# Kernel tuning notes

Measured on AMD Instinct MI355X. Metric: run time of the kernel, lower is better.

The kernel has to match this reference:

```python
import jax, jax.numpy as jnp
import numpy as np

B, L, D_IN, H, TAGS = 16, 128, 512, 256, 45


def setup_inputs() -> dict:
    key = jax.random.key(0)
    ks = jax.random.split(key, 10)
    s = 0.02
    return {
        "contextualized": jax.random.normal(ks[0], (B, L, D_IN), jnp.float32),
        "sentence_lengths": jax.random.randint(ks[1], (B,), 64, L + 1, jnp.int32),
        "desired_arcs": jax.random.randint(ks[2], (B, L), 0, L + 1, jnp.int32),
        "desired_labels": jax.random.randint(ks[3], (B, L), 0, TAGS, jnp.int32),
        "W1": jax.random.normal(ks[4], (D_IN, H), jnp.float32) * s,
        "b1": jnp.zeros((H,), jnp.float32),
        "root": jax.random.normal(ks[5], (H,), jnp.float32) * s,
        "Wp": jax.random.normal(ks[6], (2 * H, H), jnp.float32) * s,
        "bp": jnp.zeros((H,), jnp.float32),
        "W_arc": jax.random.normal(ks[7], (H, 1), jnp.float32) * s,
        "b_arc": jnp.zeros((1,), jnp.float32),
        "W_lab": jax.random.normal(ks[8], (H, TAGS), jnp.float32) * s,
        "b_lab": jnp.zeros((TAGS,), jnp.float32),
    }


def _forward(contextualized, sentence_lengths, desired_arcs, desired_labels,
             W1, b1, root, Wp, bp, W_arc, b_arc, W_lab, b_lab):
    b, l, _ = contextualized.shape
    h = W1.shape[1]
    # token representations: dense + relu
    hidden = jax.nn.relu(contextualized @ W1 + b1)                      # [B,L,H]
    # prepend learned root vector
    root_t = jnp.broadcast_to(root, (b, 1, h))
    cwr = jnp.concatenate([root_t, hidden], axis=1)                     # [B,L+1,H]
    # pairs dense: concat([tile_a, tile_b]) @ Wp == hidden@Wa + cwr@Wb (broadcast-add)
    Wa, Wb = Wp[:h], Wp[h:]
    pre = (hidden @ Wa)[:, :, None, :] + (cwr @ Wb)[:, None, :, :] + bp
    pairs_repr = jax.nn.relu(pre)                                       # [B,L,L+1,H]
    # valid-token mask from sentence lengths
    mask = (jnp.arange(l)[None, :] < sentence_lengths[:, None]).astype(jnp.float32)
    denom = jnp.maximum(mask.sum(), 1.0)
    # UAS: arc logits over L+1 head candidates, softmax CE vs gold arcs
    arc_logits = jnp.squeeze(pairs_repr @ W_arc, -1) + b_arc[0]         # [B,L,L+1]
    arc_logp = jax.nn.log_softmax(arc_logits, axis=-1)
    arc_ce = -jnp.take_along_axis(arc_logp, desired_arcs[:, :, None], axis=-1)[..., 0]
    uas_loss = jnp.sum(arc_ce * mask) / denom
    # LAS: select pair repr at gold arc, dense -> tag logits, softmax CE
    sel = jnp.take_along_axis(pairs_repr, desired_arcs[:, :, None, None].astype(jnp.int32)
                              .repeat(1, axis=2), axis=2)[:, :, 0, :]   # [B,L,H]
    label_logits = sel @ W_lab + b_lab                                  # [B,L,TAGS]
    lab_logp = jax.nn.log_softmax(label_logits, axis=-1)
    lab_ce = -jnp.take_along_axis(lab_logp, desired_labels[:, :, None], axis=-1)[..., 0]
    las_loss = jnp.sum(lab_ce * mask) / denom
    return (uas_loss + las_loss) * 0.5


def reference(contextualized, sentence_lengths, desired_arcs, desired_labels,
              W1, b1, root, Wp, bp, W_arc, b_arc, W_lab, b_lab):
    return _forward(contextualized, sentence_lengths, desired_arcs, desired_labels,
                    W1, b1, root, Wp, bp, W_arc, b_arc, W_lab, b_lab)
```

## Files before the change

### kernel.cpp

```cpp
#include <hip/hip_runtime.h>
#include <math.h>

#define NB 16
#define NL 128
#define DIN 512
#define NH 256
#define NTAGS 45
#define NM (NB*NL)
#define NJ (NL+1)

#define H_OFF     0
#define U_OFF     (2*NM*NH)
#define HV_OFF    (3*NM*NH)
#define VROOT_OFF (4*NM*NH)
#define ACC_OFF   (VROOT_OFF + NH)

__global__ __launch_bounds__(256) void gemm_hidden(
    const float* __restrict__ A,
    const float* __restrict__ W,
    const float* __restrict__ Wp,
    const float* __restrict__ root,
    float* __restrict__ h,
    float* __restrict__ vroot,
    float* __restrict__ accum)
{
    __shared__ float As[2][16][36];
    __shared__ float Bs[2][16][68];
    __shared__ float part[4][64];
    int m0 = blockIdx.x * 32;
    int n0 = blockIdx.y * 64;
    int kbase = blockIdx.z * 256;
    int tid = threadIdx.x;
    if (blockIdx.x == 0 && blockIdx.y == 0 && blockIdx.z == 0 && tid == 0) {
        accum[0] = 0.f;
        ((int*)accum)[1] = 0;
    }
    int lm = tid >> 2, lk = (tid & 3) * 4;
    int bk = tid >> 4, bn = (tid & 15) * 4;
    int tm = tid >> 4, tn = tid & 15;
    float acc[2][4] = {{0.f}};
    float4 a_r, b_r;

    auto LOADK = [&](int c) {
        int k0 = kbase + c * 16;
        if (tid < 128)
            a_r = *(const float4*)&A[(size_t)(m0 + lm) * DIN + k0 + lk];
        b_r = *(const float4*)&W[(size_t)(k0 + bk) * NH + n0 + bn];
    };
    auto WRITE = [&](int buf) {
        if (tid < 128) {
            As[buf][lk + 0][lm] = a_r.x; As[buf][lk + 1][lm] = a_r.y;
            As[buf][lk + 2][lm] = a_r.z; As[buf][lk + 3][lm] = a_r.w;
        }
        *(float4*)&Bs[buf][bk][bn] = b_r;
    };

    LOADK(0);
    WRITE(0);
    LOADK(1);
    __syncthreads();
    for (int c = 0; c < 16; ++c) {
        int buf = c & 1;
        #pragma unroll
        for (int kk = 0; kk < 16; kk++) {
            float2 a2 = *(const float2*)&As[buf][kk][tm * 2];
            float4 bv = *(const float4*)&Bs[buf][kk][tn * 4];
            float ar[2] = {a2.x, a2.y};
            float br[4] = {bv.x, bv.y, bv.z, bv.w};
            #pragma unroll
            for (int r = 0; r < 2; r++)
                #pragma unroll
                for (int cc = 0; cc < 4; cc++)
                    acc[r][cc] = fmaf(ar[r], br[cc], acc[r][cc]);
        }
        if (c < 15) {
            WRITE(buf ^ 1);
            if (c < 14) LOADK(c + 2);
            __syncthreads();
        }
    }
    float* hz = h + (size_t)blockIdx.z * NM * NH;
    int col = n0 + tn * 4;
    #pragma unroll
    for (int r = 0; r < 2; r++) {
        int row = m0 + tm * 2 + r;
        *(float4*)&hz[(size_t)row * NH + col] =
            make_float4(acc[r][0], acc[r][1], acc[r][2], acc[r][3]);
    }

    if (blockIdx.x == 63 && blockIdx.z == 1) {
        __syncthreads();
        int vcol = n0 + (tid & 63);
        int kc = tid >> 6;
        float p = 0.f;
        #pragma unroll 8
        for (int c = kc * 64; c < kc * 64 + 64; c++)
            p += root[c] * Wp[(size_t)(NH + c) * NH + vcol];
        part[kc][tid & 63] = p;
        __syncthreads();
        if (tid < 64)
            vroot[n0 + tid] = part[0][tid] + part[1][tid]
                            + part[2][tid] + part[3][tid];
    }
}

__global__ __launch_bounds__(256) void gemm_uv(
    const float* __restrict__ h,
    const float* __restrict__ b1,
    const float* __restrict__ Wp,
    const float* __restrict__ bp,
    float* __restrict__ u,
    float* __restrict__ hv)
{
    __shared__ float As[2][16][68];
    __shared__ float Bs[2][16][36];
    int m0 = blockIdx.x * 64;
    int n0 = blockIdx.y * 32;
    int tid = threadIdx.x;
    bool isU = (n0 < NH);
    int arow = tid >> 2, akq = (tid & 3) * 4;
    int bk = tid >> 3, bn = (tid & 7) * 4;
    int tm = tid >> 3, tn = tid & 7;
    float acc[2][4] = {{0.f}};
    float4 ha_r, hb_r, bi_r, b_r;

    auto LOADK = [&](int c) {
        int k0 = c * 16;
        size_t base = (size_t)(m0 + arow) * NH + k0 + akq;
        ha_r = *(const float4*)&h[base];
        hb_r = *(const float4*)&h[base + (size_t)NM * NH];
        bi_r = *(const float4*)&b1[k0 + akq];
        if (tid < 128) {
            int ck = k0 + bk;
            if (isU) b_r = *(const float4*)&Wp[(size_t)ck * NH + n0 + bn];
            else     b_r = *(const float4*)&Wp[(size_t)(NH + ck) * NH + (n0 - NH) + bn];
        }
    };
    auto WRITE = [&](int buf) {
        As[buf][akq + 0][arow] = fmaxf(ha_r.x + hb_r.x + bi_r.x, 0.f);
        As[buf][akq + 1][arow] = fmaxf(ha_r.y + hb_r.y + bi_r.y, 0.f);
        As[buf][akq + 2][arow] = fmaxf(ha_r.z + hb_r.z + bi_r.z, 0.f);
        As[buf][akq + 3][arow] = fmaxf(ha_r.w + hb_r.w + bi_r.w, 0.f);
        if (tid < 128)
            *(float4*)&Bs[buf][bk][bn] = b_r;
    };

    LOADK(0);
    WRITE(0);
    LOADK(1);
    __syncthreads();
    for (int c = 0; c < 16; ++c) {
        int buf = c & 1;
        #pragma unroll
        for (int kk = 0; kk < 16; kk++) {
            float2 a2 = *(const float2*)&As[buf][kk][tm * 2];
            float4 bv = *(const float4*)&Bs[buf][kk][tn * 4];
            float ar[2] = {a2.x, a2.y};
            float br[4] = {bv.x, bv.y, bv.z, bv.w};
            #pragma unroll
            for (int r = 0; r < 2; r++)
                #pragma unroll
                for (int cc = 0; cc < 4; cc++)
                    acc[r][cc] = fmaf(ar[r], br[cc], acc[r][cc]);
        }
        if (c < 15) {
            WRITE(buf ^ 1);
            if (c < 14) LOADK(c + 2);
            __syncthreads();
        }
    }
    if (isU) {
        int col = n0 + tn * 4;
        float4 bb = *(const float4*)&bp[col];
        #pragma unroll
        for (int r = 0; r < 2; r++) {
            int row = m0 + tm * 2 + r;
            *(float4*)&u[(size_t)row * NH + col] = make_float4(
                acc[r][0] + bb.x, acc[r][1] + bb.y,
                acc[r][2] + bb.z, acc[r][3] + bb.w);
        }
    } else {
        int col = (n0 - NH) + tn * 4;
        #pragma unroll
        for (int r = 0; r < 2; r++) {
            int row = m0 + tm * 2 + r;
            *(float4*)&hv[(size_t)row * NH + col] = make_float4(
                acc[r][0], acc[r][1], acc[r][2], acc[r][3]);
        }
    }
}

#define NBLK (NB*16)

__global__ __launch_bounds__(512) void score_loss_kernel(
    const float* __restrict__ u, const float* __restrict__ hv,
    const float* __restrict__ vroot, const float* __restrict__ W_arc,
    const float* __restrict__ W_lab, const float* __restrict__ b_lab,
    const int* __restrict__ slens, const int* __restrict__ arcs,
    const int* __restrict__ labels,
    float* __restrict__ accum, float* __restrict__ out)
{
    __shared__ float2 v2_s[32][129];
    __shared__ float2 u2_s[8][128];
    __shared__ float2 wa2_s[128];
    __shared__ float2 sel2_s[32][9];
    __shared__ float  ce_s[8];
    __shared__ int    arc_s[8], lab_s[8];

    int bb = blockIdx.x;
    int i0 = blockIdx.y * 8;
    int tid = threadIdx.x;
    int w = tid >> 6;
    int lane = tid & 63;
    int slen = slens[bb];

    if (i0 < slen) {
        {
            int r = tid >> 6, kq = (tid & 63) * 4;
            float4 a4 = *(const float4*)&u[(size_t)(bb * NL + i0 + r) * NH + kq];
            u2_s[r][(kq >> 1) + 0] = make_float2(a4.x, a4.y);
            u2_s[r][(kq >> 1) + 1] = make_float2(a4.z, a4.w);
        }
        if (tid < 128)
            wa2_s[tid] = *(const float2*)&W_arc[tid * 2];
        if (tid < 8) {
            int rg = bb * NL + i0 + tid;
            arc_s[tid] = arcs[rg];
            lab_s[tid] = labels[rg];
        }

        float4 vr[5];
        auto VLOAD = [&](int c) {
            int k0 = c * 64;
            #pragma unroll
            for (int s = 0; s < 5; ++s) {
                int idx = tid + s * 512;
                if (idx < NJ * 16) {
                    int j = idx >> 4, kq = (idx & 15) * 4;
                    const float* src = (j == 0) ? (vroot + k0 + kq)
                        : (hv + (size_t)(bb * NL + j - 1) * NH + k0 + kq);
                    vr[s] = *(const float4*)src;
                }
            }
        };
        auto VWRITE = [&]() {
            #pragma unroll
            for (int s = 0; s < 5; ++s) {
                int idx = tid + s * 512;
                if (idx < NJ * 16) {
                    int j = idx >> 4, kq = (idx & 15) * 4;
                    v2_s[(kq >> 1) + 0][j] = make_float2(vr[s].x, vr[s].y);
                    v2_s[(kq >> 1) + 1][j] = make_float2(vr[s].z, vr[s].w);
                }
            }
        };

        float acc1 = 0.f, acc2 = 0.f, s128 = 0.f, lacc = 0.f;

        VLOAD(0);
        for (int c = 0; c < 4; ++c) {
            if (c) __syncthreads();
            VWRITE();
            __syncthreads();
            if (c < 3) VLOAD(c + 1);
            int k0 = c * 64;

            __builtin_amdgcn_s_setprio(1);
            const float2* urow = u2_s[w] + (k0 >> 1);
            const float2* warow = wa2_s + (k0 >> 1);
            #pragma unroll 8
            for (int kk2 = 0; kk2 < 32; ++kk2) {
                float2 u2 = urow[kk2];
                float2 w2 = warow[kk2];
                float2 va = v2_s[kk2][lane];
                float2 vb = v2_s[kk2][lane + 64];
                acc1 += fmaxf(u2.x + va.x, 0.f) * w2.x
                      + fmaxf(u2.y + va.y, 0.f) * w2.y;
                acc2 += fmaxf(u2.x + vb.x, 0.f) * w2.x
                      + fmaxf(u2.y + vb.y, 0.f) * w2.y;
            }
            if (lane < 32) {
                float2 u2 = urow[lane];
                float2 w2 = warow[lane];
                float2 vv = v2_s[lane][128];
                s128 += fmaxf(u2.x + vv.x, 0.f) * w2.x
                      + fmaxf(u2.y + vv.y, 0.f) * w2.y;
                float2 vs = v2_s[lane][arc_s[w]];
                sel2_s[lane][w] = make_float2(fmaxf(u2.x + vs.x, 0.f),
                                              fmaxf(u2.y + vs.y, 0.f));
            }
            if (lane < NTAGS) {
                #pragma unroll 8
                for (int kk2 = 0; kk2 < 32; ++kk2) {
                    float2 s2 = sel2_s[kk2][w];
                    float w0 = W_lab[(size_t)(k0 + 2 * kk2) * NTAGS + lane];
                    float w1 = W_lab[(size_t)(k0 + 2 * kk2 + 1) * NTAGS + lane];
                    lacc = fmaf(s2.x, w0, fmaf(s2.y, w1, lacc));
                }
            }
            __builtin_amdgcn_s_setprio(0);
        }

        float s128t = s128;
        #pragma unroll
        for (int off = 32; off > 0; off >>= 1)
            s128t += __shfl_xor(s128t, off);
        float m = fmaxf(acc1, acc2);
        #pragma unroll
        for (int off = 32; off > 0; off >>= 1)
            m = fmaxf(m, __shfl_xor(m, off));
        m = fmaxf(m, s128t);
        float e = expf(acc1 - m) + expf(acc2 - m);
        #pragma unroll
        for (int off = 32; off > 0; off >>= 1)
            e += __shfl_xor(e, off);
        e += expf(s128t - m);
        int a = arc_s[w];
        float cand = (a < 64) ? acc1 : acc2;
        float s_a = __shfl(cand, a & 63, 64);
        if (a == 128) s_a = s128t;
        float arc_ce = (m + logf(e)) - s_a;

        float logit = (lane < NTAGS) ? (lacc + b_lab[lane]) : -INFINITY;
        float m2 = logit;
        #pragma unroll
        for (int off = 32; off > 0; off >>= 1)
            m2 = fmaxf(m2, __shfl_xor(m2, off));
        float e2 = (lane < NTAGS) ? expf(logit - m2) : 0.f;
        #pragma unroll
        for (int off = 32; off > 0; off >>= 1)
            e2 += __shfl_xor(e2, off);
        float l_t = __shfl(logit, lab_s[w], 64);
        float lab_ce = (m2 + logf(e2)) - l_t;

        float tot = ((i0 + w) < slen) ? (arc_ce + lab_ce) : 0.f;
        if (lane == 0) ce_s[w] = tot;
        __syncthreads();
        if (tid == 0)
            atomicAdd(accum, ce_s[0] + ce_s[1] + ce_s[2] + ce_s[3]
                           + ce_s[4] + ce_s[5] + ce_s[6] + ce_s[7]);
    }

    if (tid == 0) {
        __threadfence();
        int prev = atomicAdd((int*)accum + 1, 1);
        if (prev == NBLK - 1) {
            int d = 0;
            #pragma unroll
            for (int q = 0; q < NB; ++q) d += slens[q];
            float s = atomicAdd(accum, 0.f);
            out[0] = 0.5f * s / fmaxf((float)d, 1.f);
        }
    }
}

extern "C" void kernel_launch(void* const* d_in, const int* in_sizes, int n_in,
                              void* d_out, int out_size, void* d_ws, size_t ws_size,
                              hipStream_t stream) {
    (void)in_sizes; (void)n_in; (void)out_size; (void)ws_size;
    const float* ctx   = (const float*)d_in[0];
    const int*   slens = (const int*)  d_in[1];
    const int*   arcs  = (const int*)  d_in[2];
    const int*   labs  = (const int*)  d_in[3];
    const float* W1    = (const float*)d_in[4];
    const float* b1    = (const float*)d_in[5];
    const float* root  = (const float*)d_in[6];
    const float* Wp    = (const float*)d_in[7];
    const float* bp    = (const float*)d_in[8];
    const float* W_arc = (const float*)d_in[9];
    const float* W_lab = (const float*)d_in[11];
    const float* b_lab = (const float*)d_in[12];
    float* out = (float*)d_out;

    float* ws    = (float*)d_ws;
    float* h     = ws + H_OFF;
    float* u     = ws + U_OFF;
    float* hv    = ws + HV_OFF;
    float* vroot = ws + VROOT_OFF;
    float* accum = ws + ACC_OFF;

    gemm_hidden<<<dim3(64, 4, 2), 256, 0, stream>>>(ctx, W1, Wp, root, h, vroot, accum);
    gemm_uv<<<dim3(32, 16), 256, 0, stream>>>(h, b1, Wp, bp, u, hv);
    score_loss_kernel<<<dim3(NB, 16), 512, 0, stream>>>(
        u, hv, vroot, W_arc, W_lab, b_lab, slens, arcs, labs, accum, out);
}
```

Before: 130.1 us.

## Stage full head-vector tile in LDS once instead of chunked register prefetch

The score kernel now loads the whole [129 x 256] head-side tile (hv plus the root vector) into shared memory in a single pass. It then runs all four k-chunks of the arc/label computation without any intermediate barriers. This replaces the previous scheme, which staged 64-wide k-chunks through registers with a barrier pair per chunk. The aim is to remove the repeated synchronisation and the re-indexing overhead. In exchange, global loads no longer overlap with compute, and shared memory per block grows to roughly 140 KB, which limits each CU to one resident block.

```diff
diff --git a/kernel.cpp b/kernel.cpp
--- a/kernel.cpp
+++ b/kernel.cpp
@@ -200,7 +200,7 @@
     const int* __restrict__ labels,
     float* __restrict__ accum, float* __restrict__ out)
 {
-    __shared__ float2 v2_s[32][129];
+    __shared__ float2 v2_s[128][129];
     __shared__ float2 u2_s[8][128];
     __shared__ float2 wa2_s[128];
     __shared__ float2 sel2_s[32][9];
@@ -229,51 +229,45 @@
             lab_s[tid] = labels[rg];
         }
 
-        float4 vr[5];
-        auto VLOAD = [&](int c) {
+        {
+            int jo  = lane >> 4;
+            int kf0 = lane & 15;
+            #pragma unroll
+            for (int sj = 0; sj < 4; ++sj) {
+                int j = sj * 32 + w * 4 + jo;
+                const float* src = hv + (size_t)(bb * NL + j) * NH;
+                #pragma unroll
+                for (int sk = 0; sk < 4; ++sk) {
+                    int kf = sk * 16 + kf0;
+                    float4 t4 = *(const float4*)&src[kf * 4];
+                    v2_s[2 * kf + 0][j + 1] = make_float2(t4.x, t4.y);
+                    v2_s[2 * kf + 1][j + 1] = make_float2(t4.z, t4.w);
+                }
+            }
+            if (w == 0) {
+                float4 t4 = *(const float4*)&vroot[lane * 4];
+                v2_s[2 * lane + 0][0] = make_float2(t4.x, t4.y);
+                v2_s[2 * lane + 1][0] = make_float2(t4.z, t4.w);
+            }
+        }
+        __syncthreads();
+
+        float acc1 = 0.f, acc2 = 0.f, s128 = 0.f, lacc = 0.f;
+
+        __builtin_amdgcn_s_setprio(1);
+        #pragma unroll
+        for (int c = 0; c < 4; ++c) {
             int k0 = c * 64;
-            #pragma unroll
-            for (int s = 0; s < 5; ++s) {
-                int idx = tid + s * 512;
-                if (idx < NJ * 16) {
-                    int j = idx >> 4, kq = (idx & 15) * 4;
-                    const float* src = (j == 0) ? (vroot + k0 + kq)
-                        : (hv + (size_t)(bb * NL + j - 1) * NH + k0 + kq);
-                    vr[s] = *(const float4*)src;
-                }
-            }
-        };
-        auto VWRITE = [&]() {
-            #pragma unroll
-            for (int s = 0; s < 5; ++s) {
-                int idx = tid + s * 512;
-                if (idx < NJ * 16) {
-                    int j = idx >> 4, kq = (idx & 15) * 4;
-                    v2_s[(kq >> 1) + 0][j] = make_float2(vr[s].x, vr[s].y);
-                    v2_s[(kq >> 1) + 1][j] = make_float2(vr[s].z, vr[s].w);
-                }
-            }
-        };
-
-        float acc1 = 0.f, acc2 = 0.f, s128 = 0.f, lacc = 0.f;
-
-        VLOAD(0);
-        for (int c = 0; c < 4; ++c) {
-            if (c) __syncthreads();
-            VWRITE();
-            __syncthreads();
-            if (c < 3) VLOAD(c + 1);
-            int k0 = c * 64;
-
-            __builtin_amdgcn_s_setprio(1);
-            const float2* urow = u2_s[w] + (k0 >> 1);
-            const float2* warow = wa2_s + (k0 >> 1);
+            int kb = k0 >> 1;
+            const float2* urow = u2_s[w] + kb;
+            const float2* warow = wa2_s + kb;
+
             #pragma unroll 8
             for (int kk2 = 0; kk2 < 32; ++kk2) {
                 float2 u2 = urow[kk2];
                 float2 w2 = warow[kk2];
-                float2 va = v2_s[kk2][lane];
-                float2 vb = v2_s[kk2][lane + 64];
+                float2 va = v2_s[kb + kk2][lane];
+                float2 vb = v2_s[kb + kk2][lane + 64];
                 acc1 += fmaxf(u2.x + va.x, 0.f) * w2.x
                       + fmaxf(u2.y + va.y, 0.f) * w2.y;
                 acc2 += fmaxf(u2.x + vb.x, 0.f) * w2.x
@@ -282,10 +276,10 @@
             if (lane < 32) {
                 float2 u2 = urow[lane];
                 float2 w2 = warow[lane];
-                float2 vv = v2_s[lane][128];
+                float2 vv = v2_s[kb + lane][128];
                 s128 += fmaxf(u2.x + vv.x, 0.f) * w2.x
                       + fmaxf(u2.y + vv.y, 0.f) * w2.y;
-                float2 vs = v2_s[lane][arc_s[w]];
+                float2 vs = v2_s[kb + lane][arc_s[w]];
                 sel2_s[lane][w] = make_float2(fmaxf(u2.x + vs.x, 0.f),
                                               fmaxf(u2.y + vs.y, 0.f));
             }
@@ -298,8 +292,8 @@
                     lacc = fmaf(s2.x, w0, fmaf(s2.y, w1, lacc));
                 }
             }
-            __builtin_amdgcn_s_setprio(0);
-        }
+        }
+        __builtin_amdgcn_s_setprio(0);
 
         float s128t = s128;
         #pragma unroll
```

Result: no change. 128.9 us (-0.9%).
